# Kernel tuning notes

Hardware: AMD Instinct MI355X
Metric: run time of the kernel (lower is better)

The kernel has to match this reference:

```python
import jax, jax.numpy as jnp
import numpy as np

B, C, H, W = 8, 128, 256, 256
D = 64            # embed_dim
S = 32            # max_segments


def setup_inputs() -> dict:
    key = jax.random.key(0)
    ks = jax.random.split(key, 8)
    return {
        "segment_labels": jax.random.randint(ks[0], (B, 1, H, W), 0, S, dtype=jnp.int32),
        "features": jax.random.normal(ks[1], (B, C, H, W), jnp.float32),
        # 1x1 conv stack feat_proj: Conv2d(C->D), ReLU, Conv2d(D->D)
        "conv1_w": jax.random.normal(ks[2], (D, C), jnp.float32) * 0.05,
        "conv1_b": jnp.zeros((D,), jnp.float32),
        "conv2_w": jax.random.normal(ks[3], (D, D), jnp.float32) * 0.1,
        "conv2_b": jnp.zeros((D,), jnp.float32),
        # nn.Embedding(max_segments + 1, embed_dim)
        "embed_table": jax.random.normal(ks[4], (S + 1, D), jnp.float32) * 0.02,
        # nn.Linear(2*D, D): y = x @ W.T + b, W is (out, in)
        "out_w": jax.random.normal(ks[5], (D, 2 * D), jnp.float32) * 0.05,
        "out_b": jnp.zeros((D,), jnp.float32),
    }


def reference(segment_labels, features, conv1_w, conv1_b, conv2_w, conv2_b,
              embed_table, out_w, out_b):
    Bb, Cc, Hh, Ww = features.shape
    P = Hh * Ww
    Smax = embed_table.shape[0] - 1  # max_segments

    # feat_proj: two 1x1 convs == per-pixel GEMMs
    x = features.reshape(Bb, Cc, P)                                   # (B,C,P)
    h1 = jnp.maximum(jnp.einsum('oc,bcp->bpo', conv1_w, x) + conv1_b, 0.0)  # (B,P,D)
    feat = jnp.einsum('od,bpd->bpo', conv2_w, h1) + conv2_b           # (B,P,D)

    # Per-(batch, segment-id) masked mean via a single segment-sum pass.
    labels = segment_labels[:, 0].reshape(Bb, P)                       # (B,P) in [0,S)
    ids = (labels + Smax * jnp.arange(Bb, dtype=labels.dtype)[:, None]).reshape(-1)
    sums = jax.ops.segment_sum(feat.reshape(Bb * P, -1), ids,
                               num_segments=Bb * Smax).reshape(Bb, Smax, -1)
    counts = jax.ops.segment_sum(jnp.ones((Bb * P,), feat.dtype), ids,
                                 num_segments=Bb * Smax).reshape(Bb, Smax)
    pooled = sums / jnp.maximum(counts, 1.0)[..., None]                # (B,S,D) (zeros where absent)

    # type embedding for seg_id s (already in [0,S), clamp is a no-op but faithful)
    type_emb = embed_table[jnp.clip(jnp.arange(Smax), 0, Smax)]        # (S,D)
    combined = jnp.concatenate(
        [pooled, jnp.broadcast_to(type_emb, (Bb, Smax, type_emb.shape[-1]))], axis=-1)
    combined = jnp.einsum('oe,bse->bso', out_w, combined) + out_b      # (B,S,D)

    # torch.unique returns sorted present labels; compact present segments to the
    # front (rank order), pad rest with zeros.
    present = counts > 0                                               # (B,S)
    rank = jnp.cumsum(present.astype(jnp.int32), axis=1) - 1
    dst = jnp.where(present, rank, Smax)                               # Smax = dropped slot
    bidx = jnp.broadcast_to(jnp.arange(Bb)[:, None], (Bb, Smax))
    out = jnp.zeros_like(combined)
    out = out.at[bidx, dst].set(combined, mode='drop')
    return out
```

## Files before the change

kernel.cpp:

```cpp
#include <hip/hip_runtime.h>


#define B_ 8
#define C_ 128
#define P_ 65536
#define D_ 64
#define S_ 32
#define TM 256
#define KC 32
#define NCH (C_ / KC)

typedef short  bf16x8 __attribute__((ext_vector_type(8)));
typedef float  f32x4  __attribute__((ext_vector_type(4)));

__device__ __forceinline__ short f2bf(float f) {
  union { float f; unsigned u; } v; v.f = f;
  unsigned r = v.u + 0x7fffu + ((v.u >> 16) & 1u);
  return (short)(r >> 16);
}

__device__ __forceinline__ void gload16(const float* g, float* l) {
  __builtin_amdgcn_global_load_lds(
      (const __attribute__((address_space(1))) void*)g,
      (__attribute__((address_space(3))) void*)l, 16, 0, 0);
}

__global__ __launch_bounds__(256) void w1_to_bf16(const float* __restrict__ w1,
                                                  short* __restrict__ wbf) {
  int i = blockIdx.x * 256 + threadIdx.x;
  if (i < C_ * D_) wbf[i] = f2bf(w1[i]);
}

__global__ __launch_bounds__(256, 2) void proj_mfma(
    const int* __restrict__ labels, const float* __restrict__ feat,
    const short* __restrict__ wbf, const float* __restrict__ b1,
    float* __restrict__ gsum, int* __restrict__ gcnt)
{
  __shared__ __align__(16) float lds_x[2][KC * TM];
  __shared__ float s_acc[S_][68];
  __shared__ int   s_cnt[S_];

  const int tid  = threadIdx.x;
  const int wave = tid >> 6, l = tid & 63, m = l & 15, g = l >> 4;
  const int b    = blockIdx.y;
  const int px0  = blockIdx.x * TM;

  for (int i = tid; i < S_ * 68; i += 256) ((float*)s_acc)[i] = 0.f;
  if (tid < S_) s_cnt[tid] = 0;
  __syncthreads();

  const float* xb = feat + (size_t)b * C_ * P_ + px0;
  const int lane4 = l * 4;

  #pragma unroll
  for (int i = 0; i < 8; ++i)
    gload16(xb + (size_t)(wave * 8 + i) * P_ + lane4,
            &lds_x[0][(wave * 8 + i) * TM]);

  f32x4 acc[4][4];
  #pragma unroll
  for (int t = 0; t < 4; ++t)
    #pragma unroll
    for (int nt = 0; nt < 4; ++nt) acc[t][nt] = (f32x4){0.f, 0.f, 0.f, 0.f};

  #pragma unroll
  for (int kc = 0; kc < NCH; ++kc) {
    bf16x8 bw[4];
    #pragma unroll
    for (int nt = 0; nt < 4; ++nt)
      bw[nt] = *(const bf16x8*)&wbf[(nt * 16 + m) * C_ + kc * KC + g * 8];

    if (kc + 1 < NCH) {
      #pragma unroll
      for (int i = 0; i < 8; ++i)
        gload16(xb + (size_t)((kc + 1) * KC + wave * 8 + i) * P_ + lane4,
                &lds_x[(kc + 1) & 1][(wave * 8 + i) * TM]);
      asm volatile("s_waitcnt vmcnt(8)" ::: "memory");
    } else {
      asm volatile("s_waitcnt vmcnt(0)" ::: "memory");
    }
    __builtin_amdgcn_s_barrier();
    asm volatile("" ::: "memory");

    const float* bp = lds_x[kc & 1];
    #pragma unroll
    for (int t = 0; t < 4; ++t) {
      const int bpx = wave * 64 + t * 16 + m;
      bf16x8 af;
      #pragma unroll
      for (int j = 0; j < 8; ++j)
        af[j] = f2bf(bp[(g * 8 + j) * TM + bpx]);
      #pragma unroll
      for (int nt = 0; nt < 4; ++nt)
        acc[t][nt] = __builtin_amdgcn_mfma_f32_16x16x32_bf16(af, bw[nt],
                                                             acc[t][nt], 0, 0, 0);
    }
    asm volatile("s_waitcnt lgkmcnt(0)" ::: "memory");
    __builtin_amdgcn_sched_barrier(0);
    __builtin_amdgcn_s_barrier();
  }

  float b1v[4];
  #pragma unroll
  for (int nt = 0; nt < 4; ++nt) b1v[nt] = b1[nt * 16 + m];

  const int* lb = labels + (size_t)b * P_ + px0;
  #pragma unroll
  for (int t = 0; t < 4; ++t) {
    const int4 lv = *(const int4*)&lb[wave * 64 + t * 16 + g * 4];
    #pragma unroll
    for (int nt = 0; nt < 4; ++nt) {
      #pragma unroll
      for (int r = 0; r < 4; ++r) {
        const int lab = ((r & 2) ? ((r & 1) ? lv.w : lv.z)
                                 : ((r & 1) ? lv.y : lv.x)) & (S_ - 1);
        const float v = fmaxf(acc[t][nt][r] + b1v[nt], 0.f);
        atomicAdd(&s_acc[lab][nt * 16 + m], v);
      }
    }
    if (m < 4) {
      const int lab = ((m & 2) ? ((m & 1) ? lv.w : lv.z)
                               : ((m & 1) ? lv.y : lv.x)) & (S_ - 1);
      atomicAdd(&s_cnt[lab], 1);
    }
  }

  __syncthreads();
  for (int i = tid; i < S_ * D_; i += 256)
    atomicAdd(&gsum[(size_t)b * S_ * D_ + i], s_acc[i >> 6][i & 63]);
  if (tid < S_) atomicAdd(&gcnt[b * S_ + tid], s_cnt[tid]);
}

__global__ __launch_bounds__(64) void seg_finalize2(
    const float* __restrict__ gsum, const int* __restrict__ gcnt,
    const float* __restrict__ w2, const float* __restrict__ b2,
    const float* __restrict__ emb, const float* __restrict__ wo,
    const float* __restrict__ bo, float* __restrict__ out)
{
  const int s = blockIdx.x, b = blockIdx.y, o = threadIdx.x;
  const int co = (o < S_) ? gcnt[b * S_ + o] : 0;
  const unsigned long long mask = __ballot(co > 0);
  const int cnt = gcnt[b * S_ + s];
  if (cnt <= 0) return;
  const int rank = __popcll(mask & ((1ull << s) - 1ull));

  __shared__ float s_mean[D_], s_pool[D_];
  s_mean[o] = gsum[((size_t)b * S_ + s) * D_ + o] * (1.f / (float)cnt);
  __syncthreads();
  float pooled = b2[o];
  #pragma unroll
  for (int d = 0; d < D_; ++d) pooled += w2[o * D_ + d] * s_mean[d];
  s_pool[o] = pooled;
  __syncthreads();
  float r = bo[o];
  #pragma unroll
  for (int e = 0; e < D_; ++e) r += wo[o * 2 * D_ + e] * s_pool[e];
  #pragma unroll
  for (int e = 0; e < D_; ++e) r += wo[o * 2 * D_ + D_ + e] * emb[s * D_ + e];
  out[((size_t)b * S_ + rank) * D_ + o] = r;
}

extern "C" void kernel_launch(void* const* d_in, const int* in_sizes, int n_in,
                              void* d_out, int out_size, void* d_ws, size_t ws_size,
                              hipStream_t stream) {
  const int*   labels = (const int*)  d_in[0];
  const float* feat   = (const float*)d_in[1];
  const float* w1     = (const float*)d_in[2];
  const float* b1     = (const float*)d_in[3];
  const float* w2     = (const float*)d_in[4];
  const float* b2     = (const float*)d_in[5];
  const float* emb    = (const float*)d_in[6];
  const float* wo     = (const float*)d_in[7];
  const float* bo     = (const float*)d_in[8];
  float* out = (float*)d_out;

  char* w = (char*)d_ws;
  float* gsum = (float*)w;   w += (size_t)B_ * S_ * D_ * 4;
  int*   gcnt = (int*)w;     w += (size_t)B_ * S_ * 4;
  short* wbf  = (short*)w;

  hipMemsetAsync(d_ws, 0, (size_t)B_ * S_ * D_ * 4 + (size_t)B_ * S_ * 4, stream);
  hipMemsetAsync(d_out, 0, (size_t)out_size * sizeof(float), stream);

  w1_to_bf16<<<(C_ * D_ + 255) / 256, 256, 0, stream>>>(w1, wbf);

  dim3 grid(P_ / TM, B_);
  proj_mfma<<<grid, 256, 0, stream>>>(labels, feat, wbf, b1, gsum, gcnt);
  seg_finalize2<<<dim3(S_, B_), 64, 0, stream>>>(gsum, gcnt, w2, b2, emb, wo, bo, out);
}
```

Baseline: 233.6 us.

## Replace LDS-staged feature loads with direct vectorized register loads per wave

The projection kernel no longer stages feature tiles through LDS with async global-to-LDS loads and barriers. Each wave now loads float4 pixel quads per channel straight into registers, converts them to bf16, and reorders the mapping so that MFMA rows correspond to strided pixels. All W1 fragments are preloaded into registers and each block covers 512 pixels. This removes LDS traffic and block-wide barriers, at the cost of higher register pressure and no explicit prefetch overlap.

```diff
diff --git a/kernel.cpp b/kernel.cpp
--- a/kernel.cpp
+++ b/kernel.cpp
@@ -6,24 +6,15 @@
 #define P_ 65536
 #define D_ 64
 #define S_ 32
-#define TM 256
-#define KC 32
-#define NCH (C_ / KC)
 
-typedef short  bf16x8 __attribute__((ext_vector_type(8)));
-typedef float  f32x4  __attribute__((ext_vector_type(4)));
+typedef short bf16x8 __attribute__((ext_vector_type(8)));
+typedef float f32x4  __attribute__((ext_vector_type(4)));
 
-__device__ __forceinline__ short f2bf(float f) {
+__device__ __forceinline__ unsigned f2bfu(float f) {
   union { float f; unsigned u; } v; v.f = f;
-  unsigned r = v.u + 0x7fffu + ((v.u >> 16) & 1u);
-  return (short)(r >> 16);
+  return (v.u + 0x7fffu + ((v.u >> 16) & 1u)) >> 16;
 }
-
-__device__ __forceinline__ void gload16(const float* g, float* l) {
-  __builtin_amdgcn_global_load_lds(
-      (const __attribute__((address_space(1))) void*)g,
-      (__attribute__((address_space(3))) void*)l, 16, 0, 0);
-}
+__device__ __forceinline__ short f2bf(float f) { return (short)f2bfu(f); }
 
 __global__ __launch_bounds__(256) void w1_to_bf16(const float* __restrict__ w1,
                                                   short* __restrict__ wbf) {
@@ -31,97 +22,87 @@
   if (i < C_ * D_) wbf[i] = f2bf(w1[i]);
 }
 
-__global__ __launch_bounds__(256, 2) void proj_mfma(
+__global__ __launch_bounds__(256, 2) void proj_quad(
     const int* __restrict__ labels, const float* __restrict__ feat,
     const short* __restrict__ wbf, const float* __restrict__ b1,
     float* __restrict__ gsum, int* __restrict__ gcnt)
 {
-  __shared__ __align__(16) float lds_x[2][KC * TM];
   __shared__ float s_acc[S_][68];
   __shared__ int   s_cnt[S_];
 
-  const int tid  = threadIdx.x;
+  const int tid = threadIdx.x;
   const int wave = tid >> 6, l = tid & 63, m = l & 15, g = l >> 4;
-  const int b    = blockIdx.y;
-  const int px0  = blockIdx.x * TM;
+  const int b   = blockIdx.y;
+  const int px0 = blockIdx.x * 512 + wave * 128;
 
   for (int i = tid; i < S_ * 68; i += 256) ((float*)s_acc)[i] = 0.f;
   if (tid < S_) s_cnt[tid] = 0;
   __syncthreads();
 
-  const float* xb = feat + (size_t)b * C_ * P_ + px0;
-  const int lane4 = l * 4;
-
+  bf16x8 bfr[4][4];
   #pragma unroll
-  for (int i = 0; i < 8; ++i)
-    gload16(xb + (size_t)(wave * 8 + i) * P_ + lane4,
-            &lds_x[0][(wave * 8 + i) * TM]);
-
-  f32x4 acc[4][4];
-  #pragma unroll
-  for (int t = 0; t < 4; ++t)
+  for (int nt = 0; nt < 4; ++nt)
     #pragma unroll
-    for (int nt = 0; nt < 4; ++nt) acc[t][nt] = (f32x4){0.f, 0.f, 0.f, 0.f};
-
-  #pragma unroll
-  for (int kc = 0; kc < NCH; ++kc) {
-    bf16x8 bw[4];
-    #pragma unroll
-    for (int nt = 0; nt < 4; ++nt)
-      bw[nt] = *(const bf16x8*)&wbf[(nt * 16 + m) * C_ + kc * KC + g * 8];
-
-    if (kc + 1 < NCH) {
-      #pragma unroll
-      for (int i = 0; i < 8; ++i)
-        gload16(xb + (size_t)((kc + 1) * KC + wave * 8 + i) * P_ + lane4,
-                &lds_x[(kc + 1) & 1][(wave * 8 + i) * TM]);
-      asm volatile("s_waitcnt vmcnt(8)" ::: "memory");
-    } else {
-      asm volatile("s_waitcnt vmcnt(0)" ::: "memory");
-    }
-    __builtin_amdgcn_s_barrier();
-    asm volatile("" ::: "memory");
-
-    const float* bp = lds_x[kc & 1];
-    #pragma unroll
-    for (int t = 0; t < 4; ++t) {
-      const int bpx = wave * 64 + t * 16 + m;
-      bf16x8 af;
-      #pragma unroll
-      for (int j = 0; j < 8; ++j)
-        af[j] = f2bf(bp[(g * 8 + j) * TM + bpx]);
-      #pragma unroll
-      for (int nt = 0; nt < 4; ++nt)
-        acc[t][nt] = __builtin_amdgcn_mfma_f32_16x16x32_bf16(af, bw[nt],
-                                                             acc[t][nt], 0, 0, 0);
-    }
-    asm volatile("s_waitcnt lgkmcnt(0)" ::: "memory");
-    __builtin_amdgcn_sched_barrier(0);
-    __builtin_amdgcn_s_barrier();
-  }
-
+    for (int ks = 0; ks < 4; ++ks)
+      bfr[nt][ks] = *(const bf16x8*)&wbf[(nt * 16 + m) * C_ + ks * 32 + g * 8];
   float b1v[4];
   #pragma unroll
   for (int nt = 0; nt < 4; ++nt) b1v[nt] = b1[nt * 16 + m];
 
-  const int* lb = labels + (size_t)b * P_ + px0;
+  const int* lb = labels + (size_t)b * P_;
+  const float* xb = feat + (size_t)b * C_ * P_;
+
   #pragma unroll
-  for (int t = 0; t < 4; ++t) {
-    const int4 lv = *(const int4*)&lb[wave * 64 + t * 16 + g * 4];
+  for (int qg = 0; qg < 2; ++qg) {
+    const int qbase = px0 + qg * 64;
+
+    f32x4 acc[4][4];
     #pragma unroll
-    for (int nt = 0; nt < 4; ++nt) {
+    for (int t = 0; t < 4; ++t)
       #pragma unroll
-      for (int r = 0; r < 4; ++r) {
-        const int lab = ((r & 2) ? ((r & 1) ? lv.w : lv.z)
-                                 : ((r & 1) ? lv.y : lv.x)) & (S_ - 1);
-        const float v = fmaxf(acc[t][nt][r] + b1v[nt], 0.f);
-        atomicAdd(&s_acc[lab][nt * 16 + m], v);
+      for (int nt = 0; nt < 4; ++nt) acc[t][nt] = (f32x4){0.f, 0.f, 0.f, 0.f};
+
+    #pragma unroll
+    for (int ks = 0; ks < 4; ++ks) {
+      f32x4 xv[8];
+      #pragma unroll
+      for (int j = 0; j < 8; ++j)
+        xv[j] = *(const f32x4*)&xb[(size_t)(ks * 32 + g * 8 + j) * P_
+                                   + qbase + 4 * m];
+      bf16x8 af[4];
+      #pragma unroll
+      for (int j = 0; j < 8; ++j) {
+        af[0][j] = f2bf(xv[j][0]);
+        af[1][j] = f2bf(xv[j][1]);
+        af[2][j] = f2bf(xv[j][2]);
+        af[3][j] = f2bf(xv[j][3]);
       }
+      #pragma unroll
+      for (int t = 0; t < 4; ++t)
+        #pragma unroll
+        for (int nt = 0; nt < 4; ++nt)
+          acc[t][nt] = __builtin_amdgcn_mfma_f32_16x16x32_bf16(
+              af[t], bfr[nt][ks], acc[t][nt], 0, 0, 0);
+    }
+
+    #pragma unroll
+    for (int r = 0; r < 4; ++r) {
+      const int4 lv = *(const int4*)&lb[qbase + 4 * (g * 4 + r)];
+      const int labs[4] = { lv.x & (S_ - 1), lv.y & (S_ - 1),
+                            lv.z & (S_ - 1), lv.w & (S_ - 1) };
+      #pragma unroll
+      for (int t = 0; t < 4; ++t)
+        #pragma unroll
+        for (int nt = 0; nt < 4; ++nt)
+          atomicAdd(&s_acc[labs[t]][nt * 16 + m],
+                    fmaxf(acc[t][nt][r] + b1v[nt], 0.f));
     }
     if (m < 4) {
-      const int lab = ((m & 2) ? ((m & 1) ? lv.w : lv.z)
-                               : ((m & 1) ? lv.y : lv.x)) & (S_ - 1);
-      atomicAdd(&s_cnt[lab], 1);
+      const int4 lv = *(const int4*)&lb[qbase + 4 * (g * 4 + m)];
+      atomicAdd(&s_cnt[lv.x & (S_ - 1)], 1);
+      atomicAdd(&s_cnt[lv.y & (S_ - 1)], 1);
+      atomicAdd(&s_cnt[lv.z & (S_ - 1)], 1);
+      atomicAdd(&s_cnt[lv.w & (S_ - 1)], 1);
     }
   }
 
@@ -184,7 +165,6 @@
 
   w1_to_bf16<<<(C_ * D_ + 255) / 256, 256, 0, stream>>>(w1, wbf);
 
-  dim3 grid(P_ / TM, B_);
-  proj_mfma<<<grid, 256, 0, stream>>>(labels, feat, wbf, b1, gsum, gcnt);
+  proj_quad<<<dim3(P_ / 512, B_), 256, 0, stream>>>(labels, feat, wbf, b1, gsum, gcnt);
   seg_finalize2<<<dim3(S_, B_), 64, 0, stream>>>(gsum, gcnt, w2, b2, emb, wo, bo, out);
 }
```

New measurement: 214.3 us. 1.09x faster.
